# Optimization experiments

Measured on AMD Instinct MI355X. Metric: run time of the kernel, lower is better.

## Reference

```python
import jax, jax.numpy as jnp
import numpy as np

B, C, H, W, HEADS = 16, 512, 64, 64, 8
EPS = 1e-5


def setup_inputs() -> dict:
    key = jax.random.key(0)
    ks = jax.random.split(key, 5)
    s = C ** -0.5  # kaiming-ish scale for 1x1 conv weights
    return {
        "x": jax.random.normal(ks[0], (B, C, H, W), dtype=jnp.float32),
        "Wq": jax.random.normal(ks[1], (C, C), dtype=jnp.float32) * s,
        "Wk": jax.random.normal(ks[2], (C, C), dtype=jnp.float32) * s,
        "Wv": jax.random.normal(ks[3], (C, C), dtype=jnp.float32) * s,
        "Wo": jax.random.normal(ks[4], (C, C), dtype=jnp.float32) * s,
        "gamma": jnp.ones((C,), dtype=jnp.float32),
        "beta": jnp.zeros((C,), dtype=jnp.float32),
    }


def reference(x, Wq, Wk, Wv, Wo, gamma, beta):
    Bb, Cc, Hh, Ww = x.shape
    d = Cc // HEADS  # head_dim
    n = Hh * Ww      # number of spatial positions

    def proj(Wt):
        # 1x1 conv (no bias) == per-position channel matmul
        return jnp.einsum('oc,bchw->bohw', Wt, x).reshape(Bb, HEADS, d, n)

    q = proj(Wq)
    k = proj(Wk)
    v = proj(Wv)

    # softmax over head_dim axis (dim=-2 in the torch code)
    k = jax.nn.softmax(k, axis=-2)

    # linear attention: context = k @ v^T  -> [B, heads, d, d]
    context = jnp.einsum('bhdn,bhen->bhde', k, v)
    # out = (q^T @ context)^T -> [B, heads, d, n]
    out = jnp.einsum('bhdn,bhde->bhen', q, context)

    out = out.reshape(Bb, Cc, Hh, Ww)
    out = jnp.einsum('oc,bchw->bohw', Wo, out)

    y = out + x  # residual

    # BatchNorm2d (training-mode batch statistics, biased variance)
    mean = jnp.mean(y, axis=(0, 2, 3), keepdims=True)
    var = jnp.var(y, axis=(0, 2, 3), keepdims=True)
    yn = (y - mean) * jax.lax.rsqrt(var + EPS)
    return yn * gamma[None, :, None, None] + beta[None, :, None, None]
```

## Files before the change

kernel.cpp:

```cpp
#include <hip/hip_runtime.h>


typedef __bf16 bf16_t;
typedef bf16_t bf16x8 __attribute__((ext_vector_type(8)));
typedef float f32x4 __attribute__((ext_vector_type(4)));
typedef unsigned short u16;

__device__ __forceinline__ u16 f2bf(float f) {
    unsigned u = __builtin_bit_cast(unsigned, f);
    u += 0x7FFFu + ((u >> 16) & 1u);
    return (u16)(u >> 16);
}
__device__ __forceinline__ float bf2f(u16 h) {
    return __builtin_bit_cast(float, ((unsigned)h) << 16);
}

__device__ __forceinline__ void gload_lds16(const u16* g, u16* l) {
    __builtin_amdgcn_global_load_lds((const __attribute__((address_space(1))) void*)g,
                                     (__attribute__((address_space(3))) void*)l, 16, 0, 0);
}
__device__ __forceinline__ bf16x8 ldfrag(const u16* p) {
    return *(const bf16x8*)p;
}

__global__ __launch_bounds__(256) void cast_weights(const float* __restrict__ Wq, const float* __restrict__ Wk,
                                                    const float* __restrict__ Wv, const float* __restrict__ Wo,
                                                    u16* __restrict__ WqT, u16* __restrict__ WkB,
                                                    u16* __restrict__ WvB, u16* __restrict__ WoB) {
    int i = blockIdx.x * 256 + threadIdx.x;
    WkB[i] = f2bf(Wk[i]);
    WvB[i] = f2bf(Wv[i]);
    WoB[i] = f2bf(Wo[i]);
    int o = i >> 9, c = i & 511;
    WqT[c * 512 + o] = f2bf(Wq[i]);
}

__global__ __launch_bounds__(256) void transpose_cast(const float* __restrict__ x, u16* __restrict__ xT) {
    __shared__ u16 tile[64][65];
    int nt = blockIdx.x, ct = blockIdx.y, b = blockIdx.z;
    const float* xb = x + ((size_t)b * 512 + ct * 64) * 4096 + nt * 64;
    int t = threadIdx.x;
#pragma unroll
    for (int i = 0; i < 16; ++i) {
        int idx = i * 256 + t;
        int cl = idx >> 6, nl = idx & 63;
        tile[cl][nl] = f2bf(xb[(size_t)cl * 4096 + nl]);
    }
    __syncthreads();
    u16* xTb = xT + ((size_t)b * 4096 + nt * 64) * 512 + ct * 64;
#pragma unroll
    for (int i = 0; i < 16; ++i) {
        int idx = i * 256 + t;
        int nl = idx >> 6, cl = idx & 63;
        xTb[(size_t)nl * 512 + cl] = tile[cl][nl];
    }
}

__device__ __forceinline__ void gemm128_core(const u16* __restrict__ Ab, const u16* __restrict__ Btb,
                                             u16* Asl, u16* Bsl, f32x4 acc[4][4]) {
    const int t = threadIdx.x;
    const int l = t & 63, w = t >> 6;
    const int lrow = l & 15, lk = l >> 4;
    const int wm = w >> 1, wn = w & 1;
    const int r0 = t & 127, k40 = t >> 7;
    const int r1 = r0, k41 = k40 + 2;
    for (int kt = 0; kt < 16; ++kt) {
        const int kb = kt * 32;
        __syncthreads();
        gload_lds16(Ab + (size_t)r0 * 512 + kb + k40 * 8, Asl + t * 8);
        gload_lds16(Ab + (size_t)r1 * 512 + kb + k41 * 8, Asl + (t + 256) * 8);
        gload_lds16(Btb + (size_t)r0 * 512 + kb + k40 * 8, Bsl + t * 8);
        gload_lds16(Btb + (size_t)r1 * 512 + kb + k41 * 8, Bsl + (t + 256) * 8);
        __syncthreads();
        bf16x8 av[4], bv[4];
#pragma unroll
        for (int fi = 0; fi < 4; ++fi)
            av[fi] = ldfrag(Asl + lk * 1024 + (wm * 64 + fi * 16 + lrow) * 8);
#pragma unroll
        for (int fj = 0; fj < 4; ++fj)
            bv[fj] = ldfrag(Bsl + lk * 1024 + (wn * 64 + fj * 16 + lrow) * 8);
#pragma unroll
        for (int fi = 0; fi < 4; ++fi)
#pragma unroll
            for (int fj = 0; fj < 4; ++fj)
                acc[fi][fj] = __builtin_amdgcn_mfma_f32_16x16x32_bf16(av[fi], bv[fj], acc[fi][fj], 0, 0, 0);
    }
}

__global__ __launch_bounds__(256) void kgemm_bf16(const u16* __restrict__ A, long long sA,
                                                  const u16* __restrict__ Bt, long long sB,
                                                  u16* __restrict__ C, long long sC, int ldc, int Nt) {
    __shared__ __align__(16) u16 lds[8192];
    const int b = blockIdx.y;
    const int bm = blockIdx.x / Nt, bn = blockIdx.x % Nt;
    const u16* Ab = A + (size_t)b * sA + (size_t)bm * 128 * 512;
    const u16* Btb = Bt + (size_t)b * sB + (size_t)bn * 128 * 512;
    f32x4 acc[4][4];
#pragma unroll
    for (int i = 0; i < 4; ++i)
#pragma unroll
        for (int j = 0; j < 4; ++j) acc[i][j] = (f32x4){0.f, 0.f, 0.f, 0.f};
    gemm128_core(Ab, Btb, lds, lds + 4096, acc);
    const int t = threadIdx.x, l = t & 63, w = t >> 6;
    const int lrow = l & 15, lk = l >> 4;
    const int wm = w >> 1, wn = w & 1;
    u16* Cb = C + (size_t)b * sC;
#pragma unroll
    for (int fi = 0; fi < 4; ++fi)
#pragma unroll
        for (int fj = 0; fj < 4; ++fj)
#pragma unroll
            for (int r = 0; r < 4; ++r) {
                int m = bm * 128 + wm * 64 + fi * 16 + lk * 4 + r;
                int n = bn * 128 + wn * 64 + fj * 16 + lrow;
                Cb[(size_t)m * ldc + n] = f2bf(acc[fi][fj][r]);
            }
}

__global__ __launch_bounds__(256) void kgemm_f32res(const u16* __restrict__ A, long long sA,
                                                    const u16* __restrict__ Bt, long long sB,
                                                    const float* __restrict__ xres, float* __restrict__ y,
                                                    float* __restrict__ sums, float* __restrict__ sumsq, int Nt) {
    __shared__ __align__(16) u16 lds[8192];
    const int b = blockIdx.y;
    const int bm = blockIdx.x / Nt, bn = blockIdx.x % Nt;
    const u16* Ab = A + (size_t)b * sA + (size_t)bm * 128 * 512;
    const u16* Btb = Bt + (size_t)b * sB + (size_t)bn * 128 * 512;
    f32x4 acc[4][4];
#pragma unroll
    for (int i = 0; i < 4; ++i)
#pragma unroll
        for (int j = 0; j < 4; ++j) acc[i][j] = (f32x4){0.f, 0.f, 0.f, 0.f};
    gemm128_core(Ab, Btb, lds, lds + 4096, acc);
    const int t = threadIdx.x, l = t & 63, w = t >> 6;
    const int lrow = l & 15, lk = l >> 4;
    const int wm = w >> 1, wn = w & 1;
#pragma unroll
    for (int fi = 0; fi < 4; ++fi)
#pragma unroll
        for (int r = 0; r < 4; ++r) {
            int mg = bm * 128 + wm * 64 + fi * 16 + lk * 4 + r;
            size_t rowbase = (size_t)b * 2097152 + (size_t)mg * 4096 + bn * 128 + wn * 64;
            float rs = 0.f, rq = 0.f;
#pragma unroll
            for (int fj = 0; fj < 4; ++fj) {
                int nc = fj * 16 + lrow;
                float v = acc[fi][fj][r] + xres[rowbase + nc];
                y[rowbase + nc] = v;
                rs += v; rq += v * v;
            }
#pragma unroll
            for (int off = 1; off < 16; off <<= 1) {
                rs += __shfl_xor(rs, off);
                rq += __shfl_xor(rq, off);
            }
            if (lrow == 0) {
                atomicAdd(&sums[mg], rs);
                atomicAdd(&sumsq[mg], rq);
            }
        }
}

__global__ __launch_bounds__(256) void softmax_k(u16* __restrict__ K) {
    int gid = blockIdx.x * 256 + threadIdx.x;
    int n = gid & 4095, bh = gid >> 12;
    u16* p = K + (size_t)bh * 64 * 4096 + n;
    float v[64];
    float m = -1e30f;
#pragma unroll
    for (int d = 0; d < 64; ++d) { v[d] = bf2f(p[(size_t)d * 4096]); m = fmaxf(m, v[d]); }
    float s = 0.f;
#pragma unroll
    for (int d = 0; d < 64; ++d) { v[d] = __expf(v[d] - m); s += v[d]; }
    float inv = 1.0f / s;
#pragma unroll
    for (int d = 0; d < 64; ++d) p[(size_t)d * 4096] = f2bf(v[d] * inv);
}

__global__ __launch_bounds__(256) void ctx_partial(const u16* __restrict__ Ksm, const u16* __restrict__ V,
                                                   float* __restrict__ P) {
    __shared__ __align__(16) u16 lds[4096];
    const int bh = blockIdx.x >> 3, ks = blockIdx.x & 7;
    const u16* Ab = Ksm + (size_t)bh * 64 * 4096;
    const u16* Btb = V + (size_t)bh * 64 * 4096;
    u16* Asl = lds; u16* Bsl = lds + 2048;
    const int t = threadIdx.x, l = t & 63, w = t >> 6;
    const int lrow = l & 15, lk = l >> 4;
    const int wm = w >> 1, wn = w & 1;
    const int row = t & 63, k4 = t >> 6;
    f32x4 acc[2][2];
#pragma unroll
    for (int i = 0; i < 2; ++i)
#pragma unroll
        for (int j = 0; j < 2; ++j) acc[i][j] = (f32x4){0.f, 0.f, 0.f, 0.f};
    for (int kt = 0; kt < 16; ++kt) {
        int kb = ks * 512 + kt * 32;
        __syncthreads();
        gload_lds16(Ab + (size_t)row * 4096 + kb + k4 * 8, Asl + t * 8);
        gload_lds16(Btb + (size_t)row * 4096 + kb + k4 * 8, Bsl + t * 8);
        __syncthreads();
        bf16x8 av[2], bv[2];
#pragma unroll
        for (int fi = 0; fi < 2; ++fi)
            av[fi] = ldfrag(Asl + lk * 512 + (wm * 32 + fi * 16 + lrow) * 8);
#pragma unroll
        for (int fj = 0; fj < 2; ++fj)
            bv[fj] = ldfrag(Bsl + lk * 512 + (wn * 32 + fj * 16 + lrow) * 8);
#pragma unroll
        for (int fi = 0; fi < 2; ++fi)
#pragma unroll
            for (int fj = 0; fj < 2; ++fj)
                acc[fi][fj] = __builtin_amdgcn_mfma_f32_16x16x32_bf16(av[fi], bv[fj], acc[fi][fj], 0, 0, 0);
    }
    float* Pb = P + (size_t)blockIdx.x * 4096;
#pragma unroll
    for (int fi = 0; fi < 2; ++fi)
#pragma unroll
        for (int fj = 0; fj < 2; ++fj)
#pragma unroll
            for (int r = 0; r < 4; ++r) {
                int m = wm * 32 + fi * 16 + lk * 4 + r;
                int e = wn * 32 + fj * 16 + lrow;
                Pb[m * 64 + e] = acc[fi][fj][r];
            }
}

__global__ __launch_bounds__(256) void ctx_reduce(const float* __restrict__ P, u16* __restrict__ ctxT) {
    int gid = blockIdx.x * 256 + threadIdx.x;
    int d = gid & 63, e = (gid >> 6) & 63, bh = gid >> 12;
    const float* p = P + (size_t)bh * 8 * 4096 + d * 64 + e;
    float s = 0.f;
#pragma unroll
    for (int ks = 0; ks < 8; ++ks) s += p[(size_t)ks * 4096];
    ctxT[(size_t)bh * 4096 + e * 64 + d] = f2bf(s);
}

__global__ __launch_bounds__(256) void kgemm_wqp(const u16* __restrict__ ctxT, const u16* __restrict__ WqT,
                                                 u16* __restrict__ WqpT) {
    __shared__ __align__(16) u16 lds[4096 + 8192];
    const int nq = blockIdx.x, bh = blockIdx.y;
    const int b = bh >> 3, h = bh & 7;
    const u16* Ab = ctxT + (size_t)bh * 4096;
    const u16* Btb = WqT + (size_t)nq * 128 * 512 + h * 64;
    u16* Asl = lds; u16* Bsl = lds + 4096;
    const int t = threadIdx.x, l = t & 63, w = t >> 6;
    const int lrow = l & 15, lk = l >> 4;
    {
        int q = t;
        gload_lds16(Ab + (size_t)(q & 63) * 64 + (q >> 6) * 8, Asl + q * 8);
        q = t + 256;
        gload_lds16(Ab + (size_t)(q & 63) * 64 + (q >> 6) * 8, Asl + q * 8);
    }
#pragma unroll
    for (int i = 0; i < 4; ++i) {
        int q = t + i * 256;
        gload_lds16(Btb + (size_t)(q & 127) * 512 + (q >> 7) * 8, Bsl + q * 8);
    }
    __syncthreads();
    f32x4 acc[4][2];
#pragma unroll
    for (int i = 0; i < 4; ++i)
#pragma unroll
        for (int j = 0; j < 2; ++j) acc[i][j] = (f32x4){0.f, 0.f, 0.f, 0.f};
#pragma unroll
    for (int ksv = 0; ksv < 2; ++ksv) {
        bf16x8 av[4], bv[2];
#pragma unroll
        for (int fi = 0; fi < 4; ++fi)
            av[fi] = ldfrag(Asl + (ksv * 4 + lk) * 512 + (fi * 16 + lrow) * 8);
#pragma unroll
        for (int fj = 0; fj < 2; ++fj)
            bv[fj] = ldfrag(Bsl + (ksv * 4 + lk) * 1024 + (w * 32 + fj * 16 + lrow) * 8);
#pragma unroll
        for (int fi = 0; fi < 4; ++fi)
#pragma unroll
            for (int fj = 0; fj < 2; ++fj)
                acc[fi][fj] = __builtin_amdgcn_mfma_f32_16x16x32_bf16(av[fi], bv[fj], acc[fi][fj], 0, 0, 0);
    }
    u16* Ob = WqpT + (size_t)b * 262144 + h * 64;
#pragma unroll
    for (int fi = 0; fi < 4; ++fi)
#pragma unroll
        for (int fj = 0; fj < 2; ++fj)
#pragma unroll
            for (int r = 0; r < 4; ++r) {
                int e = fi * 16 + lk * 4 + r;
                int c = nq * 128 + w * 32 + fj * 16 + lrow;
                Ob[(size_t)c * 512 + e] = f2bf(acc[fi][fj][r]);
            }
}

__global__ void bn_finalize(const float* __restrict__ sums, const float* __restrict__ sumsq,
                            const float* __restrict__ gamma, const float* __restrict__ beta,
                            float* __restrict__ scale, float* __restrict__ shift) {
    int c = threadIdx.x;
    float inv = 1.0f / 65536.0f;
    float mean = sums[c] * inv;
    float var = sumsq[c] * inv - mean * mean;
    float rstd = rsqrtf(var + 1e-5f);
    float sc = rstd * gamma[c];
    scale[c] = sc;
    shift[c] = beta[c] - mean * sc;
}

__global__ __launch_bounds__(256) void bn_norm(float* __restrict__ y, const float* __restrict__ scale,
                                               const float* __restrict__ shift) {
    int i4 = blockIdx.x * 256 + threadIdx.x;
    float4* Y = (float4*)y;
    float4 v = Y[i4];
    int c = (i4 >> 10) & 511;
    float sc = scale[c], sh = shift[c];
    v.x = v.x * sc + sh; v.y = v.y * sc + sh; v.z = v.z * sc + sh; v.w = v.w * sc + sh;
    Y[i4] = v;
}

extern "C" void kernel_launch(void* const* d_in, const int* in_sizes, int n_in,
                              void* d_out, int out_size, void* d_ws, size_t ws_size,
                              hipStream_t stream) {
    const float* x     = (const float*)d_in[0];
    const float* Wq    = (const float*)d_in[1];
    const float* Wk    = (const float*)d_in[2];
    const float* Wv    = (const float*)d_in[3];
    const float* Wo    = (const float*)d_in[4];
    const float* gamma = (const float*)d_in[5];
    const float* beta  = (const float*)d_in[6];

    char* w = (char*)d_ws;
    u16* xT   = (u16*)(w);
    u16* Kbuf = (u16*)(w + 67108864ull);
    u16* WqT  = (u16*)(w + 134217728ull);
    u16* WkB  = WqT + 262144;
    u16* WvB  = WkB + 262144;
    u16* WoB  = WvB + 262144;
    u16* Wfin = WoB + 262144;
    float* sums  = (float*)(w + 134217728ull + 2097152ull + 8388608ull);
    float* sumsq = sums + 512;
    float* scale = sums + 1024;
    float* shift = sums + 1536;

    char* ob = (char*)d_out;
    float* ctxP = (float*)ob;
    u16* Vbuf   = (u16*)(ob + 16777216ull);
    u16* ctxT   = (u16*)(ob + 83886080ull);
    u16* WqpT   = (u16*)(ob + 84934656ull);
    float* y    = (float*)d_out;

    hipMemsetAsync(sums, 0, 4096, stream);
    cast_weights<<<1024, 256, 0, stream>>>(Wq, Wk, Wv, Wo, WqT, WkB, WvB, WoB);
    transpose_cast<<<dim3(64, 8, 16), 256, 0, stream>>>(x, xT);
    kgemm_bf16<<<dim3(128, 16), 256, 0, stream>>>(WkB, 0, xT, 2097152, Kbuf, 2097152, 4096, 32);
    kgemm_bf16<<<dim3(128, 16), 256, 0, stream>>>(WvB, 0, xT, 2097152, Vbuf, 2097152, 4096, 32);
    softmax_k<<<2048, 256, 0, stream>>>(Kbuf);
    ctx_partial<<<1024, 256, 0, stream>>>(Kbuf, Vbuf, ctxP);
    ctx_reduce<<<2048, 256, 0, stream>>>(ctxP, ctxT);
    kgemm_wqp<<<dim3(4, 128), 256, 0, stream>>>(ctxT, WqT, WqpT);
    kgemm_bf16<<<dim3(16, 16), 256, 0, stream>>>(WoB, 0, WqpT, 262144, Wfin, 262144, 512, 4);
    kgemm_f32res<<<dim3(128, 16), 256, 0, stream>>>(Wfin, 262144, xT, 2097152, x, y, sums, sumsq, 32);
    bn_finalize<<<1, 512, 0, stream>>>(sums, sumsq, gamma, beta, scale, shift);
    bn_norm<<<32768, 256, 0, stream>>>(y, scale, shift);
}
```

Measured before the change: 696.0 us.

## Double-buffer GEMM LDS loads, fuse K/V projections, store pre-BN output as bf16

Adds a double-buffered LDS pipeline to the shared GEMM core and the ctx_partial kernel, so loads for the next k-tile are issued before the current tile's MFMAs and one barrier per iteration is dropped. The K and V projections are merged into one launch that reads WkB and WvB as a single stacked weight matrix. The residual GEMM now writes y as bf16 into a workspace buffer, and bn_norm reads it and writes the float output, cutting intermediate traffic. The costs are double the LDS per block, which may lower occupancy, and bf16 rounding of y before normalization.

```diff
diff --git a/kernel.cpp b/kernel.cpp
--- a/kernel.cpp
+++ b/kernel.cpp
@@ -56,41 +56,78 @@
     }
 }
 
-__device__ __forceinline__ void gemm128_core(const u16* __restrict__ Ab, const u16* __restrict__ Btb,
-                                             u16* Asl, u16* Bsl, f32x4 acc[4][4]) {
+__device__ __forceinline__ void gemm128_dbuf(const u16* __restrict__ Ab, const u16* __restrict__ Btb,
+                                             u16* lds, f32x4 acc[4][4]) {
     const int t = threadIdx.x;
     const int l = t & 63, w = t >> 6;
     const int lrow = l & 15, lk = l >> 4;
     const int wm = w >> 1, wn = w & 1;
     const int r0 = t & 127, k40 = t >> 7;
-    const int r1 = r0, k41 = k40 + 2;
+    gload_lds16(Ab + (size_t)r0 * 512 + k40 * 8, lds + t * 8);
+    gload_lds16(Ab + (size_t)r0 * 512 + (k40 + 2) * 8, lds + (t + 256) * 8);
+    gload_lds16(Btb + (size_t)r0 * 512 + k40 * 8, lds + 4096 + t * 8);
+    gload_lds16(Btb + (size_t)r0 * 512 + (k40 + 2) * 8, lds + 4096 + (t + 256) * 8);
+    __syncthreads();
     for (int kt = 0; kt < 16; ++kt) {
-        const int kb = kt * 32;
-        __syncthreads();
-        gload_lds16(Ab + (size_t)r0 * 512 + kb + k40 * 8, Asl + t * 8);
-        gload_lds16(Ab + (size_t)r1 * 512 + kb + k41 * 8, Asl + (t + 256) * 8);
-        gload_lds16(Btb + (size_t)r0 * 512 + kb + k40 * 8, Bsl + t * 8);
-        gload_lds16(Btb + (size_t)r1 * 512 + kb + k41 * 8, Bsl + (t + 256) * 8);
-        __syncthreads();
+        const int cur = (kt & 1) << 13;
+        const int nxt = cur ^ 8192;
+        if (kt < 15) {
+            const int kb = (kt + 1) * 32;
+            gload_lds16(Ab + (size_t)r0 * 512 + kb + k40 * 8, lds + nxt + t * 8);
+            gload_lds16(Ab + (size_t)r0 * 512 + kb + (k40 + 2) * 8, lds + nxt + (t + 256) * 8);
+            gload_lds16(Btb + (size_t)r0 * 512 + kb + k40 * 8, lds + nxt + 4096 + t * 8);
+            gload_lds16(Btb + (size_t)r0 * 512 + kb + (k40 + 2) * 8, lds + nxt + 4096 + (t + 256) * 8);
+        }
         bf16x8 av[4], bv[4];
 #pragma unroll
         for (int fi = 0; fi < 4; ++fi)
-            av[fi] = ldfrag(Asl + lk * 1024 + (wm * 64 + fi * 16 + lrow) * 8);
+            av[fi] = ldfrag(lds + cur + lk * 1024 + (wm * 64 + fi * 16 + lrow) * 8);
 #pragma unroll
         for (int fj = 0; fj < 4; ++fj)
-            bv[fj] = ldfrag(Bsl + lk * 1024 + (wn * 64 + fj * 16 + lrow) * 8);
+            bv[fj] = ldfrag(lds + cur + 4096 + lk * 1024 + (wn * 64 + fj * 16 + lrow) * 8);
 #pragma unroll
         for (int fi = 0; fi < 4; ++fi)
 #pragma unroll
             for (int fj = 0; fj < 4; ++fj)
                 acc[fi][fj] = __builtin_amdgcn_mfma_f32_16x16x32_bf16(av[fi], bv[fj], acc[fi][fj], 0, 0, 0);
-    }
+        __syncthreads();
+    }
+}
+
+__global__ __launch_bounds__(256) void kgemm_kv(const u16* __restrict__ Wkv, const u16* __restrict__ xT,
+                                                u16* __restrict__ K, u16* __restrict__ V) {
+    __shared__ __align__(16) u16 lds[16384];
+    const int b = blockIdx.y;
+    const int bm = blockIdx.x >> 5, bn = blockIdx.x & 31;
+    const u16* Ab = Wkv + (size_t)bm * 128 * 512;
+    const u16* Btb = xT + (size_t)b * 2097152 + (size_t)bn * 128 * 512;
+    f32x4 acc[4][4];
+#pragma unroll
+    for (int i = 0; i < 4; ++i)
+#pragma unroll
+        for (int j = 0; j < 4; ++j) acc[i][j] = (f32x4){0.f, 0.f, 0.f, 0.f};
+    gemm128_dbuf(Ab, Btb, lds, acc);
+    const int t = threadIdx.x, l = t & 63, w = t >> 6;
+    const int lrow = l & 15, lk = l >> 4;
+    const int wm = w >> 1, wn = w & 1;
+    u16* Cb = (bm < 4) ? (K + (size_t)b * 2097152 + (size_t)bm * 128 * 4096)
+                       : (V + (size_t)b * 2097152 + (size_t)(bm - 4) * 128 * 4096);
+#pragma unroll
+    for (int fi = 0; fi < 4; ++fi)
+#pragma unroll
+        for (int fj = 0; fj < 4; ++fj)
+#pragma unroll
+            for (int r = 0; r < 4; ++r) {
+                int m = wm * 64 + fi * 16 + lk * 4 + r;
+                int n = bn * 128 + wn * 64 + fj * 16 + lrow;
+                Cb[(size_t)m * 4096 + n] = f2bf(acc[fi][fj][r]);
+            }
 }
 
 __global__ __launch_bounds__(256) void kgemm_bf16(const u16* __restrict__ A, long long sA,
                                                   const u16* __restrict__ Bt, long long sB,
                                                   u16* __restrict__ C, long long sC, int ldc, int Nt) {
-    __shared__ __align__(16) u16 lds[8192];
+    __shared__ __align__(16) u16 lds[16384];
     const int b = blockIdx.y;
     const int bm = blockIdx.x / Nt, bn = blockIdx.x % Nt;
     const u16* Ab = A + (size_t)b * sA + (size_t)bm * 128 * 512;
@@ -100,7 +137,7 @@
     for (int i = 0; i < 4; ++i)
 #pragma unroll
         for (int j = 0; j < 4; ++j) acc[i][j] = (f32x4){0.f, 0.f, 0.f, 0.f};
-    gemm128_core(Ab, Btb, lds, lds + 4096, acc);
+    gemm128_dbuf(Ab, Btb, lds, acc);
     const int t = threadIdx.x, l = t & 63, w = t >> 6;
     const int lrow = l & 15, lk = l >> 4;
     const int wm = w >> 1, wn = w & 1;
@@ -117,21 +154,20 @@
             }
 }
 
-__global__ __launch_bounds__(256) void kgemm_f32res(const u16* __restrict__ A, long long sA,
-                                                    const u16* __restrict__ Bt, long long sB,
-                                                    const float* __restrict__ xres, float* __restrict__ y,
-                                                    float* __restrict__ sums, float* __restrict__ sumsq, int Nt) {
-    __shared__ __align__(16) u16 lds[8192];
+__global__ __launch_bounds__(256) void kgemm_f32res(const u16* __restrict__ Wfin, const u16* __restrict__ xT,
+                                                    const float* __restrict__ xres, u16* __restrict__ yb,
+                                                    float* __restrict__ sums, float* __restrict__ sumsq) {
+    __shared__ __align__(16) u16 lds[16384];
     const int b = blockIdx.y;
-    const int bm = blockIdx.x / Nt, bn = blockIdx.x % Nt;
-    const u16* Ab = A + (size_t)b * sA + (size_t)bm * 128 * 512;
-    const u16* Btb = Bt + (size_t)b * sB + (size_t)bn * 128 * 512;
+    const int bm = blockIdx.x >> 5, bn = blockIdx.x & 31;
+    const u16* Ab = Wfin + (size_t)b * 262144 + (size_t)bm * 128 * 512;
+    const u16* Btb = xT + (size_t)b * 2097152 + (size_t)bn * 128 * 512;
     f32x4 acc[4][4];
 #pragma unroll
     for (int i = 0; i < 4; ++i)
 #pragma unroll
         for (int j = 0; j < 4; ++j) acc[i][j] = (f32x4){0.f, 0.f, 0.f, 0.f};
-    gemm128_core(Ab, Btb, lds, lds + 4096, acc);
+    gemm128_dbuf(Ab, Btb, lds, acc);
     const int t = threadIdx.x, l = t & 63, w = t >> 6;
     const int lrow = l & 15, lk = l >> 4;
     const int wm = w >> 1, wn = w & 1;
@@ -146,7 +182,7 @@
             for (int fj = 0; fj < 4; ++fj) {
                 int nc = fj * 16 + lrow;
                 float v = acc[fi][fj][r] + xres[rowbase + nc];
-                y[rowbase + nc] = v;
+                yb[rowbase + nc] = f2bf(v);
                 rs += v; rq += v * v;
             }
 #pragma unroll
@@ -179,11 +215,10 @@
 
 __global__ __launch_bounds__(256) void ctx_partial(const u16* __restrict__ Ksm, const u16* __restrict__ V,
                                                    float* __restrict__ P) {
-    __shared__ __align__(16) u16 lds[4096];
+    __shared__ __align__(16) u16 lds[8192];
     const int bh = blockIdx.x >> 3, ks = blockIdx.x & 7;
-    const u16* Ab = Ksm + (size_t)bh * 64 * 4096;
-    const u16* Btb = V + (size_t)bh * 64 * 4096;
-    u16* Asl = lds; u16* Bsl = lds + 2048;
+    const u16* Ab = Ksm + (size_t)bh * 262144;
+    const u16* Btb = V + (size_t)bh * 262144;
     const int t = threadIdx.x, l = t & 63, w = t >> 6;
     const int lrow = l & 15, lk = l >> 4;
     const int wm = w >> 1, wn = w & 1;
@@ -193,24 +228,30 @@
     for (int i = 0; i < 2; ++i)
 #pragma unroll
         for (int j = 0; j < 2; ++j) acc[i][j] = (f32x4){0.f, 0.f, 0.f, 0.f};
+    gload_lds16(Ab + (size_t)row * 4096 + ks * 512 + k4 * 8, lds + t * 8);
+    gload_lds16(Btb + (size_t)row * 4096 + ks * 512 + k4 * 8, lds + 2048 + t * 8);
+    __syncthreads();
     for (int kt = 0; kt < 16; ++kt) {
-        int kb = ks * 512 + kt * 32;
-        __syncthreads();
-        gload_lds16(Ab + (size_t)row * 4096 + kb + k4 * 8, Asl + t * 8);
-        gload_lds16(Btb + (size_t)row * 4096 + kb + k4 * 8, Bsl + t * 8);
-        __syncthreads();
+        const int cur = (kt & 1) << 12;
+        const int nxt = cur ^ 4096;
+        if (kt < 15) {
+            const int kb = ks * 512 + (kt + 1) * 32;
+            gload_lds16(Ab + (size_t)row * 4096 + kb + k4 * 8, lds + nxt + t * 8);
+            gload_lds16(Btb + (size_t)row * 4096 + kb + k4 * 8, lds + nxt + 2048 + t * 8);
+        }
         bf16x8 av[2], bv[2];
 #pragma unroll
         for (int fi = 0; fi < 2; ++fi)
-            av[fi] = ldfrag(Asl + lk * 512 + (wm * 32 + fi * 16 + lrow) * 8);
+            av[fi] = ldfrag(lds + cur + lk * 512 + (wm * 32 + fi * 16 + lrow) * 8);
 #pragma unroll
         for (int fj = 0; fj < 2; ++fj)
-            bv[fj] = ldfrag(Bsl + lk * 512 + (wn * 32 + fj * 16 + lrow) * 8);
+            bv[fj] = ldfrag(lds + cur + 2048 + lk * 512 + (wn * 32 + fj * 16 + lrow) * 8);
 #pragma unroll
         for (int fi = 0; fi < 2; ++fi)
 #pragma unroll
             for (int fj = 0; fj < 2; ++fj)
                 acc[fi][fj] = __builtin_amdgcn_mfma_f32_16x16x32_bf16(av[fi], bv[fj], acc[fi][fj], 0, 0, 0);
+        __syncthreads();
     }
     float* Pb = P + (size_t)blockIdx.x * 4096;
 #pragma unroll
@@ -303,15 +344,20 @@
     shift[c] = beta[c] - mean * sc;
 }
 
-__global__ __launch_bounds__(256) void bn_norm(float* __restrict__ y, const float* __restrict__ scale,
-                                               const float* __restrict__ shift) {
-    int i4 = blockIdx.x * 256 + threadIdx.x;
-    float4* Y = (float4*)y;
-    float4 v = Y[i4];
-    int c = (i4 >> 10) & 511;
+__global__ __launch_bounds__(256) void bn_norm(const u16* __restrict__ yb, const float* __restrict__ scale,
+                                               const float* __restrict__ shift, float* __restrict__ out) {
+    int i8 = blockIdx.x * 256 + threadIdx.x;
+    uint4 raw = ((const uint4*)yb)[i8];
+    int c = (i8 >> 9) & 511;
     float sc = scale[c], sh = shift[c];
-    v.x = v.x * sc + sh; v.y = v.y * sc + sh; v.z = v.z * sc + sh; v.w = v.w * sc + sh;
-    Y[i4] = v;
+    float4 o0, o1;
+    o0.x = bf2f((u16)(raw.x & 0xffff)) * sc + sh;  o0.y = bf2f((u16)(raw.x >> 16)) * sc + sh;
+    o0.z = bf2f((u16)(raw.y & 0xffff)) * sc + sh;  o0.w = bf2f((u16)(raw.y >> 16)) * sc + sh;
+    o1.x = bf2f((u16)(raw.z & 0xffff)) * sc + sh;  o1.y = bf2f((u16)(raw.z >> 16)) * sc + sh;
+    o1.z = bf2f((u16)(raw.w & 0xffff)) * sc + sh;  o1.w = bf2f((u16)(raw.w >> 16)) * sc + sh;
+    float4* O = (float4*)out;
+    O[(size_t)i8 * 2] = o0;
+    O[(size_t)i8 * 2 + 1] = o1;
 }
 
 extern "C" void kernel_launch(void* const* d_in, const int* in_sizes, int n_in,
@@ -337,25 +383,25 @@
     float* sumsq = sums + 512;
     float* scale = sums + 1024;
     float* shift = sums + 1536;
+    u16* ybuf = Kbuf;
 
     char* ob = (char*)d_out;
     float* ctxP = (float*)ob;
     u16* Vbuf   = (u16*)(ob + 16777216ull);
     u16* ctxT   = (u16*)(ob + 83886080ull);
     u16* WqpT   = (u16*)(ob + 84934656ull);
-    float* y    = (float*)d_out;
+    float* out  = (float*)d_out;
 
     hipMemsetAsync(sums, 0, 4096, stream);
     cast_weights<<<1024, 256, 0, stream>>>(Wq, Wk, Wv, Wo, WqT, WkB, WvB, WoB);
     transpose_cast<<<dim3(64, 8, 16), 256, 0, stream>>>(x, xT);
-    kgemm_bf16<<<dim3(128, 16), 256, 0, stream>>>(WkB, 0, xT, 2097152, Kbuf, 2097152, 4096, 32);
-    kgemm_bf16<<<dim3(128, 16), 256, 0, stream>>>(WvB, 0, xT, 2097152, Vbuf, 2097152, 4096, 32);
+    kgemm_kv<<<dim3(256, 16), 256, 0, stream>>>(WkB, xT, Kbuf, Vbuf);
     softmax_k<<<2048, 256, 0, stream>>>(Kbuf);
     ctx_partial<<<1024, 256, 0, stream>>>(Kbuf, Vbuf, ctxP);
     ctx_reduce<<<2048, 256, 0, stream>>>(ctxP, ctxT);
     kgemm_wqp<<<dim3(4, 128), 256, 0, stream>>>(ctxT, WqT, WqpT);
     kgemm_bf16<<<dim3(16, 16), 256, 0, stream>>>(WoB, 0, WqpT, 262144, Wfin, 262144, 512, 4);
-    kgemm_f32res<<<dim3(128, 16), 256, 0, stream>>>(Wfin, 262144, xT, 2097152, x, y, sums, sumsq, 32);
+    kgemm_f32res<<<dim3(128, 16), 256, 0, stream>>>(Wfin, xT, x, ybuf, sums, sumsq);
     bn_finalize<<<1, 512, 0, stream>>>(sums, sumsq, gamma, beta, scale, shift);
-    bn_norm<<<32768, 256, 0, stream>>>(y, scale, shift);
-}
+    bn_norm<<<16384, 256, 0, stream>>>(ybuf, scale, shift, out);
+}
```

New measurement: 675.9 us. -2.9%, faster.
